# Optimization experiments

Measured on AMD Instinct MI355X. Metric: run time of the kernel, lower is better.

Reference implementation:

```python
import jax, jax.numpy as jnp
import numpy as np

B, S, H, W, DF, D, HID, ITERS = 8, 8, 64, 64, 64, 64, 128, 3
EPS = 1e-8


def build_grid(h, w):
    ranges = [np.linspace(-1.0, 1.0, num=h), np.linspace(-1.0, 1.0, num=w)]
    g = np.meshgrid(*ranges, sparse=False, indexing='xy')
    return jnp.asarray(np.stack(g, axis=-1), dtype=jnp.float32)  # [H, W, 2]


def ln(x, g, b):
    m = jnp.mean(x, axis=-1, keepdims=True)
    v = jnp.mean((x - m) ** 2, axis=-1, keepdims=True)
    return (x - m) * jax.lax.rsqrt(v + 1e-5) * g + b


def setup_inputs() -> dict:
    key = jax.random.key(0)
    ks = iter(jax.random.split(key, 64))
    def nrm(shape, s=0.02):
        return jax.random.normal(next(ks), shape, jnp.float32) * s
    inp = {}
    inp['inputs'] = jax.random.normal(next(ks), (B, H, W, DF), jnp.float32)
    # learned slot inits and learned per-slot position / scale factors
    inp['slots_p'] = jax.random.normal(next(ks), (1, S, D), jnp.float32)
    inp['s_pos_p'] = 2.0 * jax.random.uniform(next(ks), (1, S, 2), jnp.float32) - 1.0
    inp['s_scale_p'] = 0.1 + 0.01 * jax.random.normal(next(ks), (1, S, 2), jnp.float32)
    # soft position embedding Linear(2, D)
    inp['W_pos'] = nrm((2, D)); inp['b_pos'] = jnp.zeros((D,), jnp.float32)
    # q/k/v projections
    inp['Wq'] = nrm((D, D)); inp['bq'] = jnp.zeros((D,), jnp.float32)
    inp['Wk'] = nrm((DF, D)); inp['bk'] = jnp.zeros((D,), jnp.float32)
    inp['Wv'] = nrm((DF, D)); inp['bv'] = jnp.zeros((D,), jnp.float32)
    # layernorms
    inp['g_in'] = jnp.ones((DF,), jnp.float32); inp['b_in'] = jnp.zeros((DF,), jnp.float32)
    inp['g_slots'] = jnp.ones((D,), jnp.float32); inp['b_slots'] = jnp.zeros((D,), jnp.float32)
    inp['g_k'] = jnp.ones((D,), jnp.float32); inp['b_k'] = jnp.zeros((D,), jnp.float32)
    inp['g_v'] = jnp.ones((D,), jnp.float32); inp['b_v'] = jnp.zeros((D,), jnp.float32)
    # shared kv MLP fc1_kv / fc2_kv
    inp['W1'] = nrm((D, 2 * D)); inp['b1'] = jnp.zeros((2 * D,), jnp.float32)
    inp['W2'] = nrm((2 * D, D)); inp['b2'] = jnp.zeros((D,), jnp.float32)
    # GRUCell (torch layout transposed to [in, 3*D])
    inp['W_ih'] = nrm((D, 3 * D)); inp['b_ih'] = jnp.zeros((3 * D,), jnp.float32)
    inp['W_hh'] = nrm((D, 3 * D)); inp['b_hh'] = jnp.zeros((3 * D,), jnp.float32)
    # residual slot MLP
    inp['g_pre'] = jnp.ones((D,), jnp.float32); inp['b_pre'] = jnp.zeros((D,), jnp.float32)
    inp['Wf1'] = nrm((D, HID)); inp['bf1'] = jnp.zeros((HID,), jnp.float32)
    inp['Wf2'] = nrm((HID, D)); inp['bf2'] = jnp.zeros((D,), jnp.float32)
    return inp


def reference(inputs, slots_p, s_pos_p, s_scale_p, W_pos, b_pos, Wq, bq, Wk, bk, Wv, bv,
              g_in, b_in, g_slots, b_slots, g_k, b_k, g_v, b_v, W1, b1, W2, b2,
              W_ih, W_hh, b_ih, b_hh, g_pre, b_pre, Wf1, bf1, Wf2, bf2):
    grid = build_grid(H, W)                 # [H, W, 2]
    grid_flat = grid.reshape(-1, 2)          # [HW, 2]
    scale = D ** (-0.5)

    x = ln(inputs, g_in, b_in)
    k0 = x @ Wk + bk                         # [B, H, W, D]
    v0 = x @ Wv + bv

    slots = jnp.broadcast_to(slots_p, (B, S, D))
    s_pos = jnp.clip(jnp.broadcast_to(s_pos_p, (B, S, 2)), -1.0, 1.0)[:, :, None, None, :]
    s_scale = jnp.clip(jnp.broadcast_to(s_scale_p, (B, S, 2)), 1e-3, 2.0)[:, :, None, None, :]

    def proj_kv(base, sp, ss, g, b):
        gr = (grid[None, None] - sp) / (ss * 5.0)      # [B, S, H, W, 2]
        pe = gr @ W_pos + b_pos                        # [B, S, H, W, D]
        t = (base[:, None] + pe).reshape(B, S, H * W, D)
        t = ln(t, g, b)
        return jax.nn.relu(t @ W1 + b1) @ W2 + b2      # [B, S, HW, D]

    for i in range(ITERS + 1):
        slots_prev = slots
        q = ln(slots, g_slots, b_slots) @ Wq + bq       # [B, S, D]
        kk = proj_kv(k0, s_pos, s_scale, g_k, b_k)
        vv = proj_kv(v0, s_pos, s_scale, g_v, b_v)
        dots = jnp.einsum('bid,bijd->bij', q, kk) * scale
        attn_mask = jax.nn.softmax(dots, axis=1) + EPS  # softmax over slot axis
        attn = attn_mask / jnp.sum(attn_mask, axis=-1, keepdims=True)
        updates = jnp.einsum('bijd,bij->bid', vv, attn)
        if i < ITERS:
            xg = updates.reshape(-1, D) @ W_ih + b_ih
            hg = slots_prev.reshape(-1, D) @ W_hh + b_hh
            ir, iz, inn = jnp.split(xg, 3, axis=-1)
            hr, hz, hn = jnp.split(hg, 3, axis=-1)
            r = jax.nn.sigmoid(ir + hr)
            z = jax.nn.sigmoid(iz + hz)
            n = jnp.tanh(inn + r * hn)
            slots = ((1.0 - z) * n + z * slots_prev.reshape(-1, D)).reshape(B, S, D)
            slots = slots + (jax.nn.relu(ln(slots, g_pre, b_pre) @ Wf1 + bf1) @ Wf2 + bf2)
        else:
            slots = slots_prev
        # update per-slot position / scale from the attention mask
        sp = jnp.einsum('bij,jd->bid', attn_mask, grid_flat) / jnp.sum(attn_mask, axis=-1, keepdims=True)
        diff = grid_flat[None, None] - sp[:, :, None]   # [B, S, HW, 2]
        am = attn_mask + 1e-8
        ss = jnp.sqrt(jnp.einsum('bij,bijd->bid', am, diff ** 2) / jnp.sum(am, axis=-1, keepdims=True))
        s_pos = sp[:, :, None, None, :]
        s_scale = jnp.clip(ss, 1e-3, 2.0)[:, :, None, None, :]
    return slots, s_pos, s_scale, attn_mask
```

## Files before the change

### kernel.cpp

```cpp
#include <hip/hip_runtime.h>
#include <math.h>

typedef __bf16 bf16_t;
typedef __bf16 bfrag __attribute__((ext_vector_type(8)));
typedef float ffrag __attribute__((ext_vector_type(4)));

__device__ __forceinline__ float wave_sum(float v) {
#pragma unroll
  for (int m = 32; m >= 1; m >>= 1) v += __shfl_xor(v, m, 64);
  return v;
}
__device__ __forceinline__ float lin_(int i) { return -1.f + (2.f * (float)i) / 63.f; }
__device__ __forceinline__ float bflo(unsigned u) { return __uint_as_float(u << 16); }
__device__ __forceinline__ float bfhi(unsigned u) { return __uint_as_float(u & 0xFFFF0000u); }

__global__ __launch_bounds__(256) void k_setup(
    const float* __restrict__ slots_p, const float* __restrict__ s_pos_p,
    const float* __restrict__ s_scale_p, const float* __restrict__ W1,
    const float* __restrict__ b1, const float* __restrict__ g_k,
    const float* __restrict__ b_k, const float* __restrict__ g_v,
    const float* __restrict__ b_v, const float* __restrict__ W_pos,
    const float* __restrict__ b_pos, const float* __restrict__ Wk,
    const float* __restrict__ Wv,
    float* __restrict__ slotsS, float* __restrict__ sposS,
    float* __restrict__ sscaleS, float* __restrict__ momentsHsum,
    bf16_t* __restrict__ W1kT, bf16_t* __restrict__ W1vT,
    bf16_t* __restrict__ WkT, bf16_t* __restrict__ WvT,
    float4* __restrict__ nckA, float* __restrict__ nckB,
    float4* __restrict__ ncvA, float* __restrict__ ncvB,
    float* __restrict__ possum) {
  int t = threadIdx.x;
  for (int i = t; i < 8512; i += 256) momentsHsum[i] = 0.f;
  for (int i = t; i < 4096; i += 256) slotsS[i] = slots_p[i & 511];
  if (t < 128) {
    sposS[t] = fminf(fmaxf(s_pos_p[t & 15], -1.f), 1.f);
    sscaleS[t] = fminf(fmaxf(s_scale_p[t & 15], 0.001f), 2.f);
  }
  for (int i = t; i < 4096; i += 256) {
    int n = i >> 6, d = i & 63;
    WkT[i] = (bf16_t)Wk[d * 64 + n];
    WvT[i] = (bf16_t)Wv[d * 64 + n];
  }
  if (t < 128) {
    int n = t;
    float wxk = 0, wyk = 0, wbk = 0, uk = 0, sk = 0;
    float wxv = 0, wyv = 0, wbv = 0, uv = 0, sv = 0;
    for (int c = 0; c < 64; ++c) {
      float w = W1[c * 128 + n];
      float wk = g_k[c] * w, wv = g_v[c] * w;
      W1kT[n * 64 + c] = (bf16_t)wk;
      W1vT[n * 64 + c] = (bf16_t)wv;
      float px = W_pos[c], py = W_pos[64 + c], bp = b_pos[c];
      wxk += px * wk; wyk += py * wk; wbk += bp * wk; sk += wk; uk += b_k[c] * w;
      wxv += px * wv; wyv += py * wv; wbv += bp * wv; sv += wv; uv += b_v[c] * w;
    }
    nckA[n] = make_float4(wxk, wyk, wbk, uk + b1[n]); nckB[n] = sk;
    ncvA[n] = make_float4(wxv, wyv, wbv, uv + b1[n]); ncvB[n] = sv;
  }
  if (t < 64) {
    float px = W_pos[t], py = W_pos[64 + t], bp = b_pos[t];
    float s[9] = {px, py, bp, px * px, py * py, bp * bp, px * py, px * bp, py * bp};
#pragma unroll
    for (int i = 0; i < 9; ++i) {
      float v = wave_sum(s[i]);
      if (t == 0) possum[i] = v;
    }
  }
}

__device__ __forceinline__ void pass_type(
    const bf16_t xs[][72], bf16_t t0s[][72],
    const bf16_t WTl[][72], const bf16_t W1l[][72],
    const float* __restrict__ bias, const float* wpxs, const float* wpys,
    const float* bpvs, float* __restrict__ statsG, bf16_t* __restrict__ P0G,
    int j0, int wv, int lq, int ln15) {
  ffrag C[4] = {{0,0,0,0},{0,0,0,0},{0,0,0,0},{0,0,0,0}};
#pragma unroll
  for (int ks = 0; ks < 2; ++ks) {
    bfrag a = *(const bfrag*)&xs[wv * 16 + ln15][ks * 32 + lq * 8];
#pragma unroll
    for (int nt = 0; nt < 4; ++nt) {
      bfrag bb = *(const bfrag*)&WTl[nt * 16 + ln15][ks * 32 + lq * 8];
      C[nt] = __builtin_amdgcn_mfma_f32_16x16x32_bf16(a, bb, C[nt], 0, 0, 0);
    }
  }
  float kv[4][4];
  float st[5][4];
#pragma unroll
  for (int i = 0; i < 5; ++i)
#pragma unroll
    for (int rg = 0; rg < 4; ++rg) st[i][rg] = 0.f;
#pragma unroll
  for (int nt = 0; nt < 4; ++nt) {
    int n = nt * 16 + ln15;
    float bn = bias[n], pxw = wpxs[n], pyw = wpys[n], bpw = bpvs[n];
#pragma unroll
    for (int rg = 0; rg < 4; ++rg) {
      float v = C[nt][rg] + bn;
      kv[nt][rg] = v;
      st[0][rg] += v; st[1][rg] += v * v; st[2][rg] += v * pxw;
      st[3][rg] += v * pyw; st[4][rg] += v * bpw;
    }
  }
#pragma unroll
  for (int i = 0; i < 5; ++i)
#pragma unroll
    for (int rg = 0; rg < 4; ++rg) {
      float v = st[i][rg];
      v += __shfl_xor(v, 1, 64); v += __shfl_xor(v, 2, 64);
      v += __shfl_xor(v, 4, 64); v += __shfl_xor(v, 8, 64);
      st[i][rg] = v;
    }
  if (ln15 == 0) {
#pragma unroll
    for (int rg = 0; rg < 4; ++rg) {
      int j = j0 + wv * 16 + lq * 4 + rg;
#pragma unroll
      for (int i = 0; i < 5; ++i) statsG[j * 5 + i] = st[i][rg];
    }
  }
#pragma unroll
  for (int nt = 0; nt < 4; ++nt)
#pragma unroll
    for (int rg = 0; rg < 4; ++rg)
      t0s[wv * 16 + lq * 4 + rg][nt * 16 + ln15] = (bf16_t)kv[nt][rg];
  ffrag D[8] = {{0,0,0,0},{0,0,0,0},{0,0,0,0},{0,0,0,0},
                {0,0,0,0},{0,0,0,0},{0,0,0,0},{0,0,0,0}};
#pragma unroll
  for (int ks = 0; ks < 2; ++ks) {
    bfrag a = *(const bfrag*)&t0s[wv * 16 + ln15][ks * 32 + lq * 8];
#pragma unroll
    for (int nt = 0; nt < 8; ++nt) {
      bfrag bb = *(const bfrag*)&W1l[nt * 16 + ln15][ks * 32 + lq * 8];
      D[nt] = __builtin_amdgcn_mfma_f32_16x16x32_bf16(a, bb, D[nt], 0, 0, 0);
    }
  }
#pragma unroll
  for (int nt = 0; nt < 8; ++nt)
#pragma unroll
    for (int rg = 0; rg < 4; ++rg)
      P0G[(size_t)(j0 + wv * 16 + lq * 4 + rg) * 128 + nt * 16 + ln15] =
          (bf16_t)D[nt][rg];
}

__global__ __launch_bounds__(256) void k_pre(
    const float* __restrict__ inp, const float* __restrict__ g_in,
    const float* __restrict__ b_in, const float* __restrict__ bk,
    const float* __restrict__ bv, const bf16_t* __restrict__ WkT,
    const bf16_t* __restrict__ WvT, const bf16_t* __restrict__ W1kT,
    const bf16_t* __restrict__ W1vT, const float* __restrict__ W_pos,
    const float* __restrict__ b_pos,
    bf16_t* __restrict__ P0k, bf16_t* __restrict__ P0v,
    float* __restrict__ statsK, float* __restrict__ statsV,
    const float* __restrict__ slotsS, const float* __restrict__ g_slots,
    const float* __restrict__ b_slots, const float* __restrict__ Wq,
    const float* __restrict__ bq, const float* __restrict__ W2,
    const float* __restrict__ b2, float* __restrict__ w2qg,
    float* __restrict__ b2qg) {
  __shared__ bf16_t xs[64][72];
  __shared__ bf16_t t0s[64][72];
  __shared__ bf16_t WkTl[64][72];
  __shared__ bf16_t WvTl[64][72];
  __shared__ bf16_t W1kl[128][72];
  __shared__ bf16_t W1vl[128][72];
  __shared__ float wpxs[64], wpys[64], bpvs[64];
  const int tid = threadIdx.x;
  const int j0 = blockIdx.x * 64;
  for (int i = tid; i < 512; i += 256) {
    int row = i >> 3, seg = i & 7;
    *(uint4*)&WkTl[row][seg * 8] = ((const uint4*)WkT)[i];
    *(uint4*)&WvTl[row][seg * 8] = ((const uint4*)WvT)[i];
  }
  for (int i = tid; i < 1024; i += 256) {
    int row = i >> 3, seg = i & 7;
    *(uint4*)&W1kl[row][seg * 8] = ((const uint4*)W1kT)[i];
    *(uint4*)&W1vl[row][seg * 8] = ((const uint4*)W1vT)[i];
  }
  if (tid < 64) { wpxs[tid] = W_pos[tid]; wpys[tid] = W_pos[64 + tid]; bpvs[tid] = b_pos[tid]; }
  {
    const int px = tid >> 2, cg = tid & 3;
    const float* rowp = inp + (size_t)(j0 + px) * 64 + cg * 16;
    float v[16];
    *(float4*)&v[0]  = ((const float4*)rowp)[0];
    *(float4*)&v[4]  = ((const float4*)rowp)[1];
    *(float4*)&v[8]  = ((const float4*)rowp)[2];
    *(float4*)&v[12] = ((const float4*)rowp)[3];
    float s = 0.f, s2 = 0.f;
#pragma unroll
    for (int i = 0; i < 16; ++i) { s += v[i]; s2 += v[i] * v[i]; }
    s += __shfl_xor(s, 1, 64); s += __shfl_xor(s, 2, 64);
    s2 += __shfl_xor(s2, 1, 64); s2 += __shfl_xor(s2, 2, 64);
    float m = s * 0.015625f;
    float r = rsqrtf(s2 * 0.015625f - m * m + 1e-5f);
    float g[16], bb[16];
    *(float4*)&g[0]  = ((const float4*)(g_in + cg * 16))[0];
    *(float4*)&g[4]  = ((const float4*)(g_in + cg * 16))[1];
    *(float4*)&g[8]  = ((const float4*)(g_in + cg * 16))[2];
    *(float4*)&g[12] = ((const float4*)(g_in + cg * 16))[3];
    *(float4*)&bb[0]  = ((const float4*)(b_in + cg * 16))[0];
    *(float4*)&bb[4]  = ((const float4*)(b_in + cg * 16))[1];
    *(float4*)&bb[8]  = ((const float4*)(b_in + cg * 16))[2];
    *(float4*)&bb[12] = ((const float4*)(b_in + cg * 16))[3];
#pragma unroll
    for (int e = 0; e < 8; ++e) {
      float x0 = (v[2 * e] - m) * r * g[2 * e] + bb[2 * e];
      float x1 = (v[2 * e + 1] - m) * r * g[2 * e + 1] + bb[2 * e + 1];
      union { unsigned u; bf16_t h[2]; } cv;
      cv.h[0] = (bf16_t)x0; cv.h[1] = (bf16_t)x1;
      *(unsigned*)&xs[px][cg * 16 + 2 * e] = cv.u;
    }
  }
  __syncthreads();
  const int wv = tid >> 6, lane = tid & 63, lq = lane >> 4, ln15 = lane & 15;
  pass_type(xs, t0s, WkTl, W1kl, bk, wpxs, wpys, bpvs, statsK, P0k, j0, wv, lq, ln15);
  pass_type(xs, t0s, WvTl, W1vl, bv, wpxs, wpys, bpvs, statsV, P0v, j0, wv, lq, ln15);
  if (blockIdx.x < 64 && tid < 64) {
    int bs = blockIdx.x, d = tid;
    float v = slotsS[bs * 64 + d];
    float m = wave_sum(v) * 0.015625f;
    float c = v - m;
    float var = wave_sum(c * c) * 0.015625f;
    float xn = c * rsqrtf(var + 1e-5f) * g_slots[d] + b_slots[d];
    float q = bq[d];
    for (int cc = 0; cc < 64; ++cc) q = fmaf(__shfl(xn, cc, 64), Wq[cc * 64 + d], q);
    float w0 = 0.f, w1 = 0.f;
    for (int cc = 0; cc < 64; ++cc) {
      float qc = __shfl(q, cc, 64);
      w0 = fmaf(W2[d * 64 + cc], qc, w0);
      w1 = fmaf(W2[(64 + d) * 64 + cc], qc, w1);
    }
    w2qg[bs * 128 + d] = w0;
    w2qg[bs * 128 + 64 + d] = w1;
    float p = wave_sum(b2[d] * q);
    if (d == 0) b2qg[bs] = p;
  }
}

template <int LAST>
__global__ __launch_bounds__(256) void k_iter(
    const bf16_t* __restrict__ P0kg, const bf16_t* __restrict__ P0vg,
    const float* __restrict__ statsK, const float* __restrict__ statsV,
    const float4* __restrict__ nckA, const float* __restrict__ nckB,
    const float4* __restrict__ ncvA, const float* __restrict__ ncvB,
    const float* __restrict__ possum, const float* __restrict__ w2qg,
    const float* __restrict__ b2qg, const float* __restrict__ sposS,
    const float* __restrict__ sscaleS, float* __restrict__ moments,
    float* __restrict__ Hsum, float* __restrict__ outAttn) {
  __shared__ unsigned P0kl[64 * 65];
  __shared__ unsigned P0vl[64 * 65];
  __shared__ float4 nckAl[128];
  __shared__ float nckBl[128];
  __shared__ float w2qTl[128][8];
  __shared__ float4 scalV[64][9];
  __shared__ float attnS[64][10];
  __shared__ float HsumW[4][8][128];
  __shared__ float momAcc[8][5];
  const int tid = threadIdx.x;
  const int tile = blockIdx.x, b = blockIdx.y;
  const int jg0 = b * 4096 + tile * 64;
#pragma unroll
  for (int r = 0; r < 4; ++r) {
    int idx = tid + 256 * r;
    int row = idx >> 4, seg = idx & 15;
    uint4 v = ((const uint4*)P0kg)[(size_t)(jg0 + row) * 16 + seg];
    unsigned* dst = &P0kl[row * 65 + seg * 4];
    dst[0] = v.x; dst[1] = v.y; dst[2] = v.z; dst[3] = v.w;
    if (!LAST) {
      uint4 w = ((const uint4*)P0vg)[(size_t)(jg0 + row) * 16 + seg];
      unsigned* d2 = &P0vl[row * 65 + seg * 4];
      d2[0] = w.x; d2[1] = w.y; d2[2] = w.z; d2[3] = w.w;
    }
  }
  if (tid < 128) { nckAl[tid] = nckA[tid]; nckBl[tid] = nckB[tid]; }
#pragma unroll
  for (int r = 0; r < 4; ++r) {
    int idx = tid + 256 * r;
    int s = idx >> 7, n = idx & 127;
    w2qTl[n][s] = w2qg[(b * 8 + s) * 128 + n];
  }
  if (tid < 40) momAcc[tid / 5][tid % 5] = 0.f;
  float4 ncv0 = {0, 0, 0, 0}, ncv1 = {0, 0, 0, 0};
  float wsv0 = 0.f, wsv1 = 0.f;
  if (!LAST) {
    int l = tid & 63;
    ncv0 = ncvA[l]; ncv1 = ncvA[l + 64];
    wsv0 = ncvB[l]; wsv1 = ncvB[l + 64];
  }
  __syncthreads();

  const int px = tid >> 2, sp = tid & 3;
  const int jimg = tile * 64 + px;
  const float gx = lin_(jimg & 63), gy = lin_(jimg >> 6);
  const float Swx = possum[0], Swy = possum[1], Sbp = possum[2];
  const float Swx2 = possum[3], Swy2 = possum[4], Sbp2 = possum[5];
  const float Swxy = possum[6], Swxb = possum[7], Swyb = possum[8];
  float skA[5], svA[5];
#pragma unroll
  for (int i = 0; i < 5; ++i) {
    skA[i] = statsK[(size_t)(jg0 + px) * 5 + i];
    svA[i] = statsV[(size_t)(jg0 + px) * 5 + i];
  }
  float c1a[8], c2a[8], rKa[8], mrKa[8];
#pragma unroll
  for (int s = 0; s < 8; ++s) {
    int bs = b * 8 + s;
    float spx = sposS[bs * 2], spy = sposS[bs * 2 + 1];
    float rxx = 1.f / (sscaleS[bs * 2] * 5.f);
    float ryy = 1.f / (sscaleS[bs * 2 + 1] * 5.f);
    float c1 = (gx - spx) * rxx, c2 = (gy - spy) * ryy;
    float quad = c1 * c1 * Swx2 + c2 * c2 * Swy2 + Sbp2 +
                 2.f * (c1 * c2 * Swxy + c1 * Swxb + c2 * Swyb);
    float mK = (skA[0] + c1 * Swx + c2 * Swy + Sbp) * 0.015625f;
    float e2K = (skA[1] + 2.f * (c1 * skA[2] + c2 * skA[3] + skA[4]) + quad) * 0.015625f;
    float rK = rsqrtf(e2K - mK * mK + 1e-5f);
    c1a[s] = c1; c2a[s] = c2; rKa[s] = rK; mrKa[s] = mK * rK;
    if (!LAST && (s >> 1) == sp) {
      float mV = (svA[0] + c1 * Swx + c2 * Swy + Sbp) * 0.015625f;
      float e2V = (svA[1] + 2.f * (c1 * svA[2] + c2 * svA[3] + svA[4]) + quad) * 0.015625f;
      float rV = rsqrtf(e2V - mV * mV + 1e-5f);
      scalV[px][s] = make_float4(c1, c2, rV, mV * rV);
    }
  }
  float d8[8] = {0, 0, 0, 0, 0, 0, 0, 0};
#pragma unroll 4
  for (int i = 0; i < 16; ++i) {
    int k = sp * 16 + i;
    unsigned u = P0kl[px * 65 + k];
    float p0 = bflo(u), p1 = bfhi(u);
    float4 A0 = nckAl[2 * k], A1 = nckAl[2 * k + 1];
    float ws0 = nckBl[2 * k], ws1 = nckBl[2 * k + 1];
    float4 q0a = *(const float4*)&w2qTl[2 * k][0];
    float4 q0b = *(const float4*)&w2qTl[2 * k][4];
    float4 q1a = *(const float4*)&w2qTl[2 * k + 1][0];
    float4 q1b = *(const float4*)&w2qTl[2 * k + 1][4];
    float qq0[8] = {q0a.x, q0a.y, q0a.z, q0a.w, q0b.x, q0b.y, q0b.z, q0b.w};
    float qq1[8] = {q1a.x, q1a.y, q1a.z, q1a.w, q1b.x, q1b.y, q1b.z, q1b.w};
    float bm0 = p0 + A0.z, bm1 = p1 + A1.z;
#pragma unroll
    for (int s = 0; s < 8; ++s) {
      float z0 = bm0 + c1a[s] * A0.x + c2a[s] * A0.y;
      float h0 = fmaxf(fmaf(rKa[s], z0, fmaf(-mrKa[s], ws0, A0.w)), 0.f);
      d8[s] = fmaf(h0, qq0[s], d8[s]);
      float z1 = bm1 + c1a[s] * A1.x + c2a[s] * A1.y;
      float h1 = fmaxf(fmaf(rKa[s], z1, fmaf(-mrKa[s], ws1, A1.w)), 0.f);
      d8[s] = fmaf(h1, qq1[s], d8[s]);
    }
  }
#pragma unroll
  for (int s = 0; s < 8; ++s) {
    float v = d8[s];
    v += __shfl_xor(v, 1, 64);
    v += __shfl_xor(v, 2, 64);
    d8[s] = (v + b2qg[b * 8 + s]) * 0.125f;
  }
  float mx = d8[0];
#pragma unroll
  for (int s = 1; s < 8; ++s) mx = fmaxf(mx, d8[s]);
  float tt = 0.f;
  float e8[8];
#pragma unroll
  for (int s = 0; s < 8; ++s) { e8[s] = expf(d8[s] - mx); tt += e8[s]; }
  float inv = 1.f / tt;
#pragma unroll
  for (int s = 0; s < 8; ++s) e8[s] = e8[s] * inv + 1e-8f;
  float wa, wb;
  if (sp == 0) { wa = e8[0]; wb = e8[1]; }
  else if (sp == 1) { wa = e8[2]; wb = e8[3]; }
  else if (sp == 2) { wa = e8[4]; wb = e8[5]; }
  else { wa = e8[6]; wb = e8[7]; }
  *(float2*)&attnS[px][sp * 2] = make_float2(wa, wb);
  if (LAST) {
    outAttn[(size_t)(b * 8 + sp * 2) * 4096 + jimg] = wa;
    outAttn[(size_t)(b * 8 + sp * 2 + 1) * 4096 + jimg] = wb;
  }
  {
    float mm[10] = {wa, wa * gx, wa * gy, wa * gx * gx, wa * gy * gy,
                    wb, wb * gx, wb * gy, wb * gx * gx, wb * gy * gy};
#pragma unroll
    for (int i = 0; i < 10; ++i) {
      float v = mm[i];
      v += __shfl_xor(v, 4, 64); v += __shfl_xor(v, 8, 64);
      v += __shfl_xor(v, 16, 64); v += __shfl_xor(v, 32, 64);
      mm[i] = v;
    }
    if ((tid & 63) < 4) {
#pragma unroll
      for (int i = 0; i < 5; ++i) {
        atomicAdd(&momAcc[sp * 2][i], mm[i]);
        atomicAdd(&momAcc[sp * 2 + 1][i], mm[5 + i]);
      }
    }
  }
  __syncthreads();

  if (!LAST) {
    const int w = tid >> 6, l = tid & 63;
    float hacc[8][2];
#pragma unroll
    for (int s = 0; s < 8; ++s) { hacc[s][0] = 0.f; hacc[s][1] = 0.f; }
    const unsigned short* P16 = (const unsigned short*)P0vl;
#pragma unroll 2
    for (int i = 0; i < 16; ++i) {
      int j = w * 16 + i;
      float pv0 = __uint_as_float((unsigned)P16[j * 130 + l] << 16);
      float pv1 = __uint_as_float((unsigned)P16[j * 130 + 64 + l] << 16);
      float bm0 = pv0 + ncv0.z, bm1 = pv1 + ncv1.z;
#pragma unroll
      for (int s = 0; s < 8; ++s) {
        float4 sc = scalV[j][s];
        float aw = attnS[j][s];
        float z0 = bm0 + sc.x * ncv0.x + sc.y * ncv0.y;
        float h0 = fmaxf(fmaf(sc.z, z0, fmaf(-sc.w, wsv0, ncv0.w)), 0.f);
        hacc[s][0] = fmaf(aw, h0, hacc[s][0]);
        float z1 = bm1 + sc.x * ncv1.x + sc.y * ncv1.y;
        float h1 = fmaxf(fmaf(sc.z, z1, fmaf(-sc.w, wsv1, ncv1.w)), 0.f);
        hacc[s][1] = fmaf(aw, h1, hacc[s][1]);
      }
    }
#pragma unroll
    for (int s = 0; s < 8; ++s) {
      HsumW[w][s][l] = hacc[s][0];
      HsumW[w][s][l + 64] = hacc[s][1];
    }
    __syncthreads();
#pragma unroll
    for (int r = 0; r < 4; ++r) {
      int i = tid + 256 * r;
      int s = i >> 7, n = i & 127;
      float v = HsumW[0][s][n] + HsumW[1][s][n] + HsumW[2][s][n] + HsumW[3][s][n];
      atomicAdd(&Hsum[(b * 8 + s) * 128 + n], v);
    }
  }
  if (tid < 40)
    atomicAdd(&moments[(b * 8 + tid / 5) * 5 + tid % 5], momAcc[tid / 5][tid % 5]);
}

__global__ __launch_bounds__(192) void k_fin(
    float* __restrict__ moments, float* __restrict__ Hsum,
    const float* __restrict__ W2, const float* __restrict__ b2,
    const float* __restrict__ W_ih, const float* __restrict__ b_ih,
    const float* __restrict__ W_hh, const float* __restrict__ b_hh,
    const float* __restrict__ g_pre, const float* __restrict__ b_pre,
    const float* __restrict__ Wf1, const float* __restrict__ bf1,
    const float* __restrict__ Wf2, const float* __restrict__ bf2,
    const float* __restrict__ g_slots, const float* __restrict__ b_slots,
    const float* __restrict__ Wq, const float* __restrict__ bq,
    float* __restrict__ slotsS, float* __restrict__ sposS, float* __restrict__ sscaleS,
    float* __restrict__ w2qg, float* __restrict__ b2qg,
    float* __restrict__ outSlots, float* __restrict__ outSpos,
    float* __restrict__ outSscale, int last) {
  const int bs = blockIdx.x;
  const int t = threadIdx.x;
  __shared__ float hsum_s[128], upd[64], sprev[64], xg[192], hg[192];
  __shared__ float snew[64], xpre[64], hf[128], sfin[64], xn[64], qsh[64];
  const float M0 = moments[bs * 5 + 0];
  const float M1x = moments[bs * 5 + 1], M1y = moments[bs * 5 + 2];
  const float M2x = moments[bs * 5 + 3], M2y = moments[bs * 5 + 4];
  const float invM0 = 1.f / M0;
  const float spx = M1x * invM0, spy = M1y * invM0;
  const float M0a = M0 + 4096.f * 1e-8f;
  const float G2 = 1408.6772487f * 1e-8f;
  const float vx = (M2x + G2 - 2.f * spx * M1x + spx * spx * M0a) / M0a;
  const float vy = (M2y + G2 - 2.f * spy * M1y + spy * spy * M0a) / M0a;
  float ssx = sqrtf(fmaxf(vx, 0.f)), ssy = sqrtf(fmaxf(vy, 0.f));
  ssx = fminf(fmaxf(ssx, 0.001f), 2.f);
  ssy = fminf(fmaxf(ssy, 0.001f), 2.f);
  if (t == 0) {
    sposS[bs * 2 + 0] = spx; sposS[bs * 2 + 1] = spy;
    sscaleS[bs * 2 + 0] = ssx; sscaleS[bs * 2 + 1] = ssy;
    if (last) {
      outSpos[bs * 2 + 0] = spx; outSpos[bs * 2 + 1] = spy;
      outSscale[bs * 2 + 0] = ssx; outSscale[bs * 2 + 1] = ssy;
    }
  }
  if (last) {
    if (t < 64) outSlots[bs * 64 + t] = slotsS[bs * 64 + t];
    return;
  }
  if (t < 128) hsum_s[t] = Hsum[bs * 128 + t];
  if (t < 64) sprev[t] = slotsS[bs * 64 + t];
  __syncthreads();
  if (t < 128) Hsum[bs * 128 + t] = 0.f;
  if (t < 5) moments[bs * 5 + t] = 0.f;
  if (t < 64) {
    float a = 0.f;
#pragma unroll
    for (int k = 0; k < 128; ++k) a += hsum_s[k] * W2[k * 64 + t];
    upd[t] = a * invM0 + b2[t];
  }
  __syncthreads();
  {
    float a = b_ih[t], h = b_hh[t];
#pragma unroll
    for (int d = 0; d < 64; ++d) {
      a += upd[d] * W_ih[d * 192 + t];
      h += sprev[d] * W_hh[d * 192 + t];
    }
    xg[t] = a; hg[t] = h;
  }
  __syncthreads();
  if (t < 64) {
    float r = 1.f / (1.f + expf(-(xg[t] + hg[t])));
    float z = 1.f / (1.f + expf(-(xg[64 + t] + hg[64 + t])));
    float n = tanhf(xg[128 + t] + r * hg[128 + t]);
    snew[t] = (1.f - z) * n + z * sprev[t];
  }
  __syncthreads();
  if (t < 64) {
    float v = snew[t];
    float m = wave_sum(v) * 0.015625f;
    float c = v - m;
    float var = wave_sum(c * c) * 0.015625f;
    xpre[t] = c * rsqrtf(var + 1e-5f) * g_pre[t] + b_pre[t];
  }
  __syncthreads();
  if (t < 128) {
    float a = bf1[t];
#pragma unroll
    for (int d = 0; d < 64; ++d) a += xpre[d] * Wf1[d * 128 + t];
    hf[t] = fmaxf(a, 0.f);
  }
  __syncthreads();
  if (t < 64) {
    float a = bf2[t];
#pragma unroll
    for (int k = 0; k < 128; ++k) a += hf[k] * Wf2[k * 64 + t];
    float nv = snew[t] + a;
    slotsS[bs * 64 + t] = nv;
    sfin[t] = nv;
  }
  __syncthreads();
  if (t < 64) {
    float v = sfin[t];
    float m = wave_sum(v) * 0.015625f;
    float c = v - m;
    float var = wave_sum(c * c) * 0.015625f;
    xn[t] = c * rsqrtf(var + 1e-5f) * g_slots[t] + b_slots[t];
  }
  __syncthreads();
  if (t < 64) {
    float a = bq[t];
#pragma unroll
    for (int d = 0; d < 64; ++d) a += xn[d] * Wq[d * 64 + t];
    qsh[t] = a;
  }
  __syncthreads();
  if (t < 128) {
    float a = 0.f;
#pragma unroll
    for (int d = 0; d < 64; ++d) a += W2[t * 64 + d] * qsh[d];
    w2qg[bs * 128 + t] = a;
  }
  if (t < 64) {
    float p = wave_sum(b2[t] * qsh[t]);
    if (t == 0) b2qg[bs] = p;
  }
}

extern "C" void kernel_launch(void* const* d_in, const int* in_sizes, int n_in,
                              void* d_out, int out_size, void* d_ws, size_t ws_size,
                              hipStream_t stream) {
  const float* const* in = (const float* const*)d_in;
  float* ws = (float*)d_ws;
  bf16_t* P0k   = (bf16_t*)(ws + 0);
  bf16_t* P0v   = (bf16_t*)(ws + 2097152);
  float* statsK = ws + 4194304;
  float* statsV = ws + 4358144;
  float* w2qg   = ws + 4521984;
  float* b2qg   = ws + 4530176;
  float* slotsS = ws + 4530240;
  float* sposS  = ws + 4534336;
  float* sscaleS= ws + 4534464;
  float* moments= ws + 4534592;
  float* Hsum   = ws + 4534912;
  bf16_t* W1kT  = (bf16_t*)(ws + 4543104);
  bf16_t* W1vT  = (bf16_t*)(ws + 4547200);
  bf16_t* WkT   = (bf16_t*)(ws + 4551296);
  bf16_t* WvT   = (bf16_t*)(ws + 4553344);
  float4* nckA  = (float4*)(ws + 4555392);
  float* nckB   = ws + 4555904;
  float4* ncvA  = (float4*)(ws + 4556032);
  float* ncvB   = ws + 4556544;
  float* possum = ws + 4556672;

  float* out = (float*)d_out;
  float* outSlots  = out;
  float* outSpos   = out + 4096;
  float* outSscale = out + 4224;
  float* outAttn   = out + 4352;

  k_setup<<<1, 256, 0, stream>>>(in[1], in[2], in[3], in[20], in[21],
                                 in[16], in[17], in[18], in[19], in[4], in[5],
                                 in[8], in[10], slotsS, sposS, sscaleS, moments,
                                 W1kT, W1vT, WkT, WvT, nckA, nckB, ncvA, ncvB, possum);
  k_pre<<<512, 256, 0, stream>>>(in[0], in[12], in[13], in[9], in[11],
                                 WkT, WvT, W1kT, W1vT, in[4], in[5],
                                 P0k, P0v, statsK, statsV,
                                 slotsS, in[14], in[15], in[6], in[7], in[22], in[23],
                                 w2qg, b2qg);
  for (int i = 0; i < 4; ++i) {
    int last = (i == 3) ? 1 : 0;
    if (!last) {
      k_iter<0><<<dim3(64, 8), 256, 0, stream>>>(
          P0k, P0v, statsK, statsV, nckA, nckB, ncvA, ncvB, possum,
          w2qg, b2qg, sposS, sscaleS, moments, Hsum, outAttn);
    } else {
      k_iter<1><<<dim3(64, 8), 256, 0, stream>>>(
          P0k, P0v, statsK, statsV, nckA, nckB, ncvA, ncvB, possum,
          w2qg, b2qg, sposS, sscaleS, moments, Hsum, outAttn);
    }
    k_fin<<<64, 192, 0, stream>>>(moments, Hsum, in[22], in[23], in[24], in[25],
                                  in[26], in[27], in[28], in[29], in[30], in[31],
                                  in[32], in[33], in[14], in[15], in[6], in[7],
                                  slotsS, sposS, sscaleS, w2qg, b2qg,
                                  outSlots, outSpos, outSscale, last);
  }
}
```

Measured before the change: 300.4 us.

## Fuse setup, precompute and iteration kernels into one persistent kernel with grid barriers

Replaces the chain of setup, pre, iter and fin launches with a single persistent kernel of 256 blocks synchronised by atomic-counter grid barriers. Each block keeps its two tiles of projected K/V activations (P0k/P0v) and per-row stats in shared memory across all iterations, instead of writing them to global memory and reading them back. This removes about ten kernel launches and the global round trips of the large intermediate buffers. In exchange it relies on all blocks being co-resident, uses about 118 KB of shared memory per block, and leaves the tiny finalize step serialised on 64 blocks while the others wait at the barrier.

```diff
diff --git a/kernel.cpp b/kernel.cpp
--- a/kernel.cpp
+++ b/kernel.cpp
@@ -4,6 +4,8 @@
 typedef __bf16 bf16_t;
 typedef __bf16 bfrag __attribute__((ext_vector_type(8)));
 typedef float ffrag __attribute__((ext_vector_type(4)));
+
+#define NBLK 256u
 
 __device__ __forceinline__ float wave_sum(float v) {
 #pragma unroll
@@ -14,66 +16,53 @@
 __device__ __forceinline__ float bflo(unsigned u) { return __uint_as_float(u << 16); }
 __device__ __forceinline__ float bfhi(unsigned u) { return __uint_as_float(u & 0xFFFF0000u); }
 
-__global__ __launch_bounds__(256) void k_setup(
-    const float* __restrict__ slots_p, const float* __restrict__ s_pos_p,
-    const float* __restrict__ s_scale_p, const float* __restrict__ W1,
-    const float* __restrict__ b1, const float* __restrict__ g_k,
-    const float* __restrict__ b_k, const float* __restrict__ g_v,
-    const float* __restrict__ b_v, const float* __restrict__ W_pos,
-    const float* __restrict__ b_pos, const float* __restrict__ Wk,
-    const float* __restrict__ Wv,
-    float* __restrict__ slotsS, float* __restrict__ sposS,
-    float* __restrict__ sscaleS, float* __restrict__ momentsHsum,
-    bf16_t* __restrict__ W1kT, bf16_t* __restrict__ W1vT,
-    bf16_t* __restrict__ WkT, bf16_t* __restrict__ WvT,
-    float4* __restrict__ nckA, float* __restrict__ nckB,
-    float4* __restrict__ ncvA, float* __restrict__ ncvB,
-    float* __restrict__ possum) {
-  int t = threadIdx.x;
-  for (int i = t; i < 8512; i += 256) momentsHsum[i] = 0.f;
-  for (int i = t; i < 4096; i += 256) slotsS[i] = slots_p[i & 511];
-  if (t < 128) {
-    sposS[t] = fminf(fmaxf(s_pos_p[t & 15], -1.f), 1.f);
-    sscaleS[t] = fminf(fmaxf(s_scale_p[t & 15], 0.001f), 2.f);
-  }
-  for (int i = t; i < 4096; i += 256) {
-    int n = i >> 6, d = i & 63;
-    WkT[i] = (bf16_t)Wk[d * 64 + n];
-    WvT[i] = (bf16_t)Wv[d * 64 + n];
-  }
-  if (t < 128) {
-    int n = t;
-    float wxk = 0, wyk = 0, wbk = 0, uk = 0, sk = 0;
-    float wxv = 0, wyv = 0, wbv = 0, uv = 0, sv = 0;
-    for (int c = 0; c < 64; ++c) {
-      float w = W1[c * 128 + n];
-      float wk = g_k[c] * w, wv = g_v[c] * w;
-      W1kT[n * 64 + c] = (bf16_t)wk;
-      W1vT[n * 64 + c] = (bf16_t)wv;
-      float px = W_pos[c], py = W_pos[64 + c], bp = b_pos[c];
-      wxk += px * wk; wyk += py * wk; wbk += bp * wk; sk += wk; uk += b_k[c] * w;
-      wxv += px * wv; wyv += py * wv; wbv += bp * wv; sv += wv; uv += b_v[c] * w;
-    }
-    nckA[n] = make_float4(wxk, wyk, wbk, uk + b1[n]); nckB[n] = sk;
-    ncvA[n] = make_float4(wxv, wyv, wbv, uv + b1[n]); ncvB[n] = sv;
-  }
-  if (t < 64) {
-    float px = W_pos[t], py = W_pos[64 + t], bp = b_pos[t];
-    float s[9] = {px, py, bp, px * px, py * py, bp * bp, px * py, px * bp, py * bp};
-#pragma unroll
-    for (int i = 0; i < 9; ++i) {
-      float v = wave_sum(s[i]);
-      if (t == 0) possum[i] = v;
-    }
-  }
+__device__ __forceinline__ void gbar(unsigned* ctr) {
+  __syncthreads();
+  if (threadIdx.x == 0) {
+    __threadfence();
+    atomicAdd(ctr, 1u);
+    while (__hip_atomic_load(ctr, __ATOMIC_RELAXED, __HIP_MEMORY_SCOPE_AGENT) < NBLK)
+      __builtin_amdgcn_s_sleep(1);
+  }
+  __syncthreads();
+  __threadfence();
 }
 
+struct FinS {
+  float hsum_s[128], upd[64], sprev[64], xg[192], hg[192];
+  float snew[64], xpre[64], hf[128], sfin[64], xn[64], qsh[64];
+};
+struct SmemPre {
+  bf16_t xs[64][72];
+  bf16_t t0s[64][72];
+  bf16_t WTl[64][72];
+  bf16_t W1l[128][72];
+  float wpxs[64], wpys[64], bpvs[64];
+};
+struct SmemIter {
+  float4 nckAl[128];
+  float nckBl[128];
+  float w2qTl[128][8];
+  float4 scalV[64][9];
+  float attnS[64][10];
+  union { float HsumW[4][8][128]; FinS fin; };
+  float momAcc[8][5];
+};
+struct Smem {
+  unsigned P0kl[2][64 * 65];
+  unsigned P0vl[2][64 * 65];
+  float scr[2][640];
+  union { SmemPre pre; SmemIter it; } u;
+};
+static_assert(sizeof(Smem) == 118528, "layout");
+static_assert(sizeof(Smem) <= 163840, "fits one block per CU");
+
 __device__ __forceinline__ void pass_type(
-    const bf16_t xs[][72], bf16_t t0s[][72],
-    const bf16_t WTl[][72], const bf16_t W1l[][72],
+    const bf16_t (*xs)[72], bf16_t (*t0s)[72],
+    const bf16_t (*WTl)[72], const bf16_t (*W1l)[72],
     const float* __restrict__ bias, const float* wpxs, const float* wpys,
-    const float* bpvs, float* __restrict__ statsG, bf16_t* __restrict__ P0G,
-    int j0, int wv, int lq, int ln15) {
+    const float* bpvs, float st[5][4], unsigned* P0L,
+    int wv, int lq, int ln15) {
   ffrag C[4] = {{0,0,0,0},{0,0,0,0},{0,0,0,0},{0,0,0,0}};
 #pragma unroll
   for (int ks = 0; ks < 2; ++ks) {
@@ -85,7 +74,6 @@
     }
   }
   float kv[4][4];
-  float st[5][4];
 #pragma unroll
   for (int i = 0; i < 5; ++i)
 #pragma unroll
@@ -111,14 +99,6 @@
       v += __shfl_xor(v, 4, 64); v += __shfl_xor(v, 8, 64);
       st[i][rg] = v;
     }
-  if (ln15 == 0) {
-#pragma unroll
-    for (int rg = 0; rg < 4; ++rg) {
-      int j = j0 + wv * 16 + lq * 4 + rg;
-#pragma unroll
-      for (int i = 0; i < 5; ++i) statsG[j * 5 + i] = st[i][rg];
-    }
-  }
 #pragma unroll
   for (int nt = 0; nt < 4; ++nt)
 #pragma unroll
@@ -135,94 +115,218 @@
       D[nt] = __builtin_amdgcn_mfma_f32_16x16x32_bf16(a, bb, D[nt], 0, 0, 0);
     }
   }
+  bf16_t* P16 = (bf16_t*)P0L;
 #pragma unroll
   for (int nt = 0; nt < 8; ++nt)
 #pragma unroll
     for (int rg = 0; rg < 4; ++rg)
-      P0G[(size_t)(j0 + wv * 16 + lq * 4 + rg) * 128 + nt * 16 + ln15] =
-          (bf16_t)D[nt][rg];
+      P16[(wv * 16 + lq * 4 + rg) * 130 + nt * 16 + ln15] = (bf16_t)D[nt][rg];
 }
 
-__global__ __launch_bounds__(256) void k_pre(
-    const float* __restrict__ inp, const float* __restrict__ g_in,
-    const float* __restrict__ b_in, const float* __restrict__ bk,
-    const float* __restrict__ bv, const bf16_t* __restrict__ WkT,
-    const bf16_t* __restrict__ WvT, const bf16_t* __restrict__ W1kT,
-    const bf16_t* __restrict__ W1vT, const float* __restrict__ W_pos,
+__global__ __launch_bounds__(256) void k_fused(
+    const float* __restrict__ inp,
+    const float* __restrict__ slots_p,
+    const float* __restrict__ s_pos_p,
+    const float* __restrict__ s_scale_p,
+    const float* __restrict__ W_pos,
     const float* __restrict__ b_pos,
-    bf16_t* __restrict__ P0k, bf16_t* __restrict__ P0v,
-    float* __restrict__ statsK, float* __restrict__ statsV,
-    const float* __restrict__ slotsS, const float* __restrict__ g_slots,
-    const float* __restrict__ b_slots, const float* __restrict__ Wq,
-    const float* __restrict__ bq, const float* __restrict__ W2,
-    const float* __restrict__ b2, float* __restrict__ w2qg,
-    float* __restrict__ b2qg) {
-  __shared__ bf16_t xs[64][72];
-  __shared__ bf16_t t0s[64][72];
-  __shared__ bf16_t WkTl[64][72];
-  __shared__ bf16_t WvTl[64][72];
-  __shared__ bf16_t W1kl[128][72];
-  __shared__ bf16_t W1vl[128][72];
-  __shared__ float wpxs[64], wpys[64], bpvs[64];
+    const float* __restrict__ Wq,
+    const float* __restrict__ bq,
+    const float* __restrict__ Wk,
+    const float* __restrict__ bk,
+    const float* __restrict__ Wv,
+    const float* __restrict__ bv,
+    const float* __restrict__ g_in,
+    const float* __restrict__ b_in,
+    const float* __restrict__ g_slots,
+    const float* __restrict__ b_slots,
+    const float* __restrict__ g_k,
+    const float* __restrict__ b_k,
+    const float* __restrict__ g_v,
+    const float* __restrict__ b_v,
+    const float* __restrict__ W1,
+    const float* __restrict__ b1,
+    const float* __restrict__ W2,
+    const float* __restrict__ b2,
+    const float* __restrict__ W_ih,
+    const float* __restrict__ b_ih,
+    const float* __restrict__ W_hh,
+    const float* __restrict__ b_hh,
+    const float* __restrict__ g_pre,
+    const float* __restrict__ b_pre,
+    const float* __restrict__ Wf1,
+    const float* __restrict__ bf1,
+    const float* __restrict__ Wf2,
+    const float* __restrict__ bf2,
+    float* __restrict__ ws,
+    float* __restrict__ outSlots, float* __restrict__ outSpos,
+    float* __restrict__ outSscale, float* __restrict__ outAttn) {
+  __shared__ Smem sm;
   const int tid = threadIdx.x;
-  const int j0 = blockIdx.x * 64;
-  for (int i = tid; i < 512; i += 256) {
-    int row = i >> 3, seg = i & 7;
-    *(uint4*)&WkTl[row][seg * 8] = ((const uint4*)WkT)[i];
-    *(uint4*)&WvTl[row][seg * 8] = ((const uint4*)WvT)[i];
-  }
-  for (int i = tid; i < 1024; i += 256) {
-    int row = i >> 3, seg = i & 7;
-    *(uint4*)&W1kl[row][seg * 8] = ((const uint4*)W1kT)[i];
-    *(uint4*)&W1vl[row][seg * 8] = ((const uint4*)W1vT)[i];
-  }
-  if (tid < 64) { wpxs[tid] = W_pos[tid]; wpys[tid] = W_pos[64 + tid]; bpvs[tid] = b_pos[tid]; }
-  {
-    const int px = tid >> 2, cg = tid & 3;
-    const float* rowp = inp + (size_t)(j0 + px) * 64 + cg * 16;
-    float v[16];
-    *(float4*)&v[0]  = ((const float4*)rowp)[0];
-    *(float4*)&v[4]  = ((const float4*)rowp)[1];
-    *(float4*)&v[8]  = ((const float4*)rowp)[2];
-    *(float4*)&v[12] = ((const float4*)rowp)[3];
-    float s = 0.f, s2 = 0.f;
-#pragma unroll
-    for (int i = 0; i < 16; ++i) { s += v[i]; s2 += v[i] * v[i]; }
-    s += __shfl_xor(s, 1, 64); s += __shfl_xor(s, 2, 64);
-    s2 += __shfl_xor(s2, 1, 64); s2 += __shfl_xor(s2, 2, 64);
-    float m = s * 0.015625f;
-    float r = rsqrtf(s2 * 0.015625f - m * m + 1e-5f);
-    float g[16], bb[16];
-    *(float4*)&g[0]  = ((const float4*)(g_in + cg * 16))[0];
-    *(float4*)&g[4]  = ((const float4*)(g_in + cg * 16))[1];
-    *(float4*)&g[8]  = ((const float4*)(g_in + cg * 16))[2];
-    *(float4*)&g[12] = ((const float4*)(g_in + cg * 16))[3];
-    *(float4*)&bb[0]  = ((const float4*)(b_in + cg * 16))[0];
-    *(float4*)&bb[4]  = ((const float4*)(b_in + cg * 16))[1];
-    *(float4*)&bb[8]  = ((const float4*)(b_in + cg * 16))[2];
-    *(float4*)&bb[12] = ((const float4*)(b_in + cg * 16))[3];
-#pragma unroll
-    for (int e = 0; e < 8; ++e) {
-      float x0 = (v[2 * e] - m) * r * g[2 * e] + bb[2 * e];
-      float x1 = (v[2 * e + 1] - m) * r * g[2 * e + 1] + bb[2 * e + 1];
-      union { unsigned u; bf16_t h[2]; } cv;
-      cv.h[0] = (bf16_t)x0; cv.h[1] = (bf16_t)x1;
-      *(unsigned*)&xs[px][cg * 16 + 2 * e] = cv.u;
-    }
-  }
-  __syncthreads();
+  const int bid = blockIdx.x;
+  const int tl = bid & 63;
+  const int b0 = bid >> 6;
+
+  float* slotsS  = ws;
+  float* sposS   = ws + 4096;
+  float* sscaleS = ws + 4224;
+  float* moments = ws + 4352;
+  float* Hsum    = ws + 4672;
+  float* w2qg    = ws + 12864;
+  float* b2qg    = ws + 21056;
+  bf16_t* W1kT   = (bf16_t*)(ws + 21120);
+  bf16_t* W1vT   = (bf16_t*)(ws + 25216);
+  bf16_t* WkT    = (bf16_t*)(ws + 29312);
+  bf16_t* WvT    = (bf16_t*)(ws + 31360);
+  float4* nckA   = (float4*)(ws + 33408);
+  float* nckB    = ws + 33920;
+  float4* ncvA   = (float4*)(ws + 34048);
+  float* ncvB    = ws + 34560;
+  float* possum  = ws + 34688;
+  unsigned* bar  = (unsigned*)(ws + 34816);
+
+  if (bid == 0) {
+    int t = tid;
+    for (int i = t; i < 8512; i += 256) moments[i] = 0.f;
+    for (int i = t; i < 4096; i += 256) slotsS[i] = slots_p[i & 511];
+    if (t < 128) {
+      sposS[t] = fminf(fmaxf(s_pos_p[t & 15], -1.f), 1.f);
+      sscaleS[t] = fminf(fmaxf(s_scale_p[t & 15], 0.001f), 2.f);
+    }
+    for (int i = t; i < 4096; i += 256) {
+      int n = i >> 6, d = i & 63;
+      WkT[i] = (bf16_t)Wk[d * 64 + n];
+      WvT[i] = (bf16_t)Wv[d * 64 + n];
+    }
+    if (t < 128) {
+      int n = t;
+      float wxk = 0, wyk = 0, wbk = 0, uk = 0, sk = 0;
+      float wxv = 0, wyv = 0, wbv = 0, uv = 0, sv = 0;
+      for (int c = 0; c < 64; ++c) {
+        float w = W1[c * 128 + n];
+        float wkk = g_k[c] * w, wvv = g_v[c] * w;
+        W1kT[n * 64 + c] = (bf16_t)wkk;
+        W1vT[n * 64 + c] = (bf16_t)wvv;
+        float pxc = W_pos[c], pyc = W_pos[64 + c], bpc = b_pos[c];
+        wxk += pxc * wkk; wyk += pyc * wkk; wbk += bpc * wkk; sk += wkk; uk += b_k[c] * w;
+        wxv += pxc * wvv; wyv += pyc * wvv; wbv += bpc * wvv; sv += wvv; uv += b_v[c] * w;
+      }
+      nckA[n] = make_float4(wxk, wyk, wbk, uk + b1[n]); nckB[n] = sk;
+      ncvA[n] = make_float4(wxv, wyv, wbv, uv + b1[n]); ncvB[n] = sv;
+    }
+    if (t < 64) {
+      float pxc = W_pos[t], pyc = W_pos[64 + t], bpc = b_pos[t];
+      float s9[9] = {pxc, pyc, bpc, pxc * pxc, pyc * pyc, bpc * bpc,
+                     pxc * pyc, pxc * bpc, pyc * bpc};
+#pragma unroll
+      for (int i = 0; i < 9; ++i) {
+        float v = wave_sum(s9[i]);
+        if (t == 0) possum[i] = v;
+      }
+    }
+  }
+  gbar(&bar[0]);
+
   const int wv = tid >> 6, lane = tid & 63, lq = lane >> 4, ln15 = lane & 15;
-  pass_type(xs, t0s, WkTl, W1kl, bk, wpxs, wpys, bpvs, statsK, P0k, j0, wv, lq, ln15);
-  pass_type(xs, t0s, WvTl, W1vl, bv, wpxs, wpys, bpvs, statsV, P0v, j0, wv, lq, ln15);
-  if (blockIdx.x < 64 && tid < 64) {
-    int bs = blockIdx.x, d = tid;
+  for (int u = 0; u < 2; ++u) {
+    const int j0 = (bid + u * 256) * 64;
+    {
+      const int pxl = tid >> 2, cgl = tid & 3;
+      const float* rowp = inp + (size_t)(j0 + pxl) * 64 + cgl * 16;
+      float v[16];
+      *(float4*)&v[0]  = ((const float4*)rowp)[0];
+      *(float4*)&v[4]  = ((const float4*)rowp)[1];
+      *(float4*)&v[8]  = ((const float4*)rowp)[2];
+      *(float4*)&v[12] = ((const float4*)rowp)[3];
+      float s = 0.f, s2 = 0.f;
+#pragma unroll
+      for (int i = 0; i < 16; ++i) { s += v[i]; s2 += v[i] * v[i]; }
+      s += __shfl_xor(s, 1, 64); s += __shfl_xor(s, 2, 64);
+      s2 += __shfl_xor(s2, 1, 64); s2 += __shfl_xor(s2, 2, 64);
+      float m = s * 0.015625f;
+      float r = rsqrtf(s2 * 0.015625f - m * m + 1e-5f);
+      float g[16], bb[16];
+      *(float4*)&g[0]  = ((const float4*)(g_in + cgl * 16))[0];
+      *(float4*)&g[4]  = ((const float4*)(g_in + cgl * 16))[1];
+      *(float4*)&g[8]  = ((const float4*)(g_in + cgl * 16))[2];
+      *(float4*)&g[12] = ((const float4*)(g_in + cgl * 16))[3];
+      *(float4*)&bb[0]  = ((const float4*)(b_in + cgl * 16))[0];
+      *(float4*)&bb[4]  = ((const float4*)(b_in + cgl * 16))[1];
+      *(float4*)&bb[8]  = ((const float4*)(b_in + cgl * 16))[2];
+      *(float4*)&bb[12] = ((const float4*)(b_in + cgl * 16))[3];
+#pragma unroll
+      for (int e = 0; e < 8; ++e) {
+        float x0 = (v[2 * e] - m) * r * g[2 * e] + bb[2 * e];
+        float x1 = (v[2 * e + 1] - m) * r * g[2 * e + 1] + bb[2 * e + 1];
+        union { unsigned uu; bf16_t h[2]; } cv;
+        cv.h[0] = (bf16_t)x0; cv.h[1] = (bf16_t)x1;
+        *(unsigned*)&sm.u.pre.xs[pxl][cgl * 16 + 2 * e] = cv.uu;
+      }
+    }
+    if (u == 0 && tid < 64) {
+      sm.u.pre.wpxs[tid] = W_pos[tid];
+      sm.u.pre.wpys[tid] = W_pos[64 + tid];
+      sm.u.pre.bpvs[tid] = b_pos[tid];
+    }
+    for (int i = tid; i < 512; i += 256) {
+      int row = i >> 3, seg = i & 7;
+      *(uint4*)&sm.u.pre.WTl[row][seg * 8] = ((const uint4*)WkT)[i];
+    }
+    for (int i = tid; i < 1024; i += 256) {
+      int row = i >> 3, seg = i & 7;
+      *(uint4*)&sm.u.pre.W1l[row][seg * 8] = ((const uint4*)W1kT)[i];
+    }
+    __syncthreads();
+    float stK[5][4], stV[5][4];
+    pass_type(sm.u.pre.xs, sm.u.pre.t0s, sm.u.pre.WTl, sm.u.pre.W1l, bk,
+              sm.u.pre.wpxs, sm.u.pre.wpys, sm.u.pre.bpvs, stK, sm.P0kl[u],
+              wv, lq, ln15);
+    __syncthreads();
+    for (int i = tid; i < 512; i += 256) {
+      int row = i >> 3, seg = i & 7;
+      *(uint4*)&sm.u.pre.WTl[row][seg * 8] = ((const uint4*)WvT)[i];
+    }
+    for (int i = tid; i < 1024; i += 256) {
+      int row = i >> 3, seg = i & 7;
+      *(uint4*)&sm.u.pre.W1l[row][seg * 8] = ((const uint4*)W1vT)[i];
+    }
+    __syncthreads();
+    pass_type(sm.u.pre.xs, sm.u.pre.t0s, sm.u.pre.WTl, sm.u.pre.W1l, bv,
+              sm.u.pre.wpxs, sm.u.pre.wpys, sm.u.pre.bpvs, stV, sm.P0vl[u],
+              wv, lq, ln15);
+    if (ln15 == 0) {
+#pragma unroll
+      for (int rg = 0; rg < 4; ++rg) {
+        int row = wv * 16 + lq * 4 + rg;
+#pragma unroll
+        for (int i = 0; i < 5; ++i) {
+          sm.scr[u][row * 5 + i] = stK[i][rg];
+          sm.scr[u][320 + row * 5 + i] = stV[i][rg];
+        }
+      }
+    }
+    __syncthreads();
+  }
+
+  if (tid < 128) { sm.u.it.nckAl[tid] = nckA[tid]; sm.u.it.nckBl[tid] = nckB[tid]; }
+  float4 ncv0, ncv1; float wsv0, wsv1;
+  { int l = tid & 63; ncv0 = ncvA[l]; ncv1 = ncvA[l + 64]; wsv0 = ncvB[l]; wsv1 = ncvB[l + 64]; }
+  const float Swx = possum[0], Swy = possum[1], Sbp = possum[2];
+  const float Swx2 = possum[3], Swy2 = possum[4], Sbp2 = possum[5];
+  const float Swxy = possum[6], Swxb = possum[7], Swyb = possum[8];
+  const int px = tid >> 2, sp = tid & 3;
+  const int jimg = tl * 64 + px;
+  const float gx = lin_(px), gy = lin_(tl);
+
+  if (bid < 64 && tid < 64) {
+    int bs = bid, d = tid;
     float v = slotsS[bs * 64 + d];
     float m = wave_sum(v) * 0.015625f;
     float c = v - m;
     float var = wave_sum(c * c) * 0.015625f;
-    float xn = c * rsqrtf(var + 1e-5f) * g_slots[d] + b_slots[d];
+    float xnv = c * rsqrtf(var + 1e-5f) * g_slots[d] + b_slots[d];
     float q = bq[d];
-    for (int cc = 0; cc < 64; ++cc) q = fmaf(__shfl(xn, cc, 64), Wq[cc * 64 + d], q);
+    for (int cc = 0; cc < 64; ++cc) q = fmaf(__shfl(xnv, cc, 64), Wq[cc * 64 + d], q);
     float w0 = 0.f, w1 = 0.f;
     for (int cc = 0; cc < 64; ++cc) {
       float qc = __shfl(q, cc, 64);
@@ -234,385 +338,297 @@
     float p = wave_sum(b2[d] * q);
     if (d == 0) b2qg[bs] = p;
   }
-}
-
-template <int LAST>
-__global__ __launch_bounds__(256) void k_iter(
-    const bf16_t* __restrict__ P0kg, const bf16_t* __restrict__ P0vg,
-    const float* __restrict__ statsK, const float* __restrict__ statsV,
-    const float4* __restrict__ nckA, const float* __restrict__ nckB,
-    const float4* __restrict__ ncvA, const float* __restrict__ ncvB,
-    const float* __restrict__ possum, const float* __restrict__ w2qg,
-    const float* __restrict__ b2qg, const float* __restrict__ sposS,
-    const float* __restrict__ sscaleS, float* __restrict__ moments,
-    float* __restrict__ Hsum, float* __restrict__ outAttn) {
-  __shared__ unsigned P0kl[64 * 65];
-  __shared__ unsigned P0vl[64 * 65];
-  __shared__ float4 nckAl[128];
-  __shared__ float nckBl[128];
-  __shared__ float w2qTl[128][8];
-  __shared__ float4 scalV[64][9];
-  __shared__ float attnS[64][10];
-  __shared__ float HsumW[4][8][128];
-  __shared__ float momAcc[8][5];
-  const int tid = threadIdx.x;
-  const int tile = blockIdx.x, b = blockIdx.y;
-  const int jg0 = b * 4096 + tile * 64;
-#pragma unroll
-  for (int r = 0; r < 4; ++r) {
-    int idx = tid + 256 * r;
-    int row = idx >> 4, seg = idx & 15;
-    uint4 v = ((const uint4*)P0kg)[(size_t)(jg0 + row) * 16 + seg];
-    unsigned* dst = &P0kl[row * 65 + seg * 4];
-    dst[0] = v.x; dst[1] = v.y; dst[2] = v.z; dst[3] = v.w;
-    if (!LAST) {
-      uint4 w = ((const uint4*)P0vg)[(size_t)(jg0 + row) * 16 + seg];
-      unsigned* d2 = &P0vl[row * 65 + seg * 4];
-      d2[0] = w.x; d2[1] = w.y; d2[2] = w.z; d2[3] = w.w;
-    }
-  }
-  if (tid < 128) { nckAl[tid] = nckA[tid]; nckBl[tid] = nckB[tid]; }
-#pragma unroll
-  for (int r = 0; r < 4; ++r) {
-    int idx = tid + 256 * r;
-    int s = idx >> 7, n = idx & 127;
-    w2qTl[n][s] = w2qg[(b * 8 + s) * 128 + n];
-  }
-  if (tid < 40) momAcc[tid / 5][tid % 5] = 0.f;
-  float4 ncv0 = {0, 0, 0, 0}, ncv1 = {0, 0, 0, 0};
-  float wsv0 = 0.f, wsv1 = 0.f;
-  if (!LAST) {
-    int l = tid & 63;
-    ncv0 = ncvA[l]; ncv1 = ncvA[l + 64];
-    wsv0 = ncvB[l]; wsv1 = ncvB[l + 64];
-  }
-  __syncthreads();
-
-  const int px = tid >> 2, sp = tid & 3;
-  const int jimg = tile * 64 + px;
-  const float gx = lin_(jimg & 63), gy = lin_(jimg >> 6);
-  const float Swx = possum[0], Swy = possum[1], Sbp = possum[2];
-  const float Swx2 = possum[3], Swy2 = possum[4], Sbp2 = possum[5];
-  const float Swxy = possum[6], Swxb = possum[7], Swyb = possum[8];
-  float skA[5], svA[5];
-#pragma unroll
-  for (int i = 0; i < 5; ++i) {
-    skA[i] = statsK[(size_t)(jg0 + px) * 5 + i];
-    svA[i] = statsV[(size_t)(jg0 + px) * 5 + i];
-  }
-  float c1a[8], c2a[8], rKa[8], mrKa[8];
-#pragma unroll
-  for (int s = 0; s < 8; ++s) {
-    int bs = b * 8 + s;
-    float spx = sposS[bs * 2], spy = sposS[bs * 2 + 1];
-    float rxx = 1.f / (sscaleS[bs * 2] * 5.f);
-    float ryy = 1.f / (sscaleS[bs * 2 + 1] * 5.f);
-    float c1 = (gx - spx) * rxx, c2 = (gy - spy) * ryy;
-    float quad = c1 * c1 * Swx2 + c2 * c2 * Swy2 + Sbp2 +
-                 2.f * (c1 * c2 * Swxy + c1 * Swxb + c2 * Swyb);
-    float mK = (skA[0] + c1 * Swx + c2 * Swy + Sbp) * 0.015625f;
-    float e2K = (skA[1] + 2.f * (c1 * skA[2] + c2 * skA[3] + skA[4]) + quad) * 0.015625f;
-    float rK = rsqrtf(e2K - mK * mK + 1e-5f);
-    c1a[s] = c1; c2a[s] = c2; rKa[s] = rK; mrKa[s] = mK * rK;
-    if (!LAST && (s >> 1) == sp) {
-      float mV = (svA[0] + c1 * Swx + c2 * Swy + Sbp) * 0.015625f;
-      float e2V = (svA[1] + 2.f * (c1 * svA[2] + c2 * svA[3] + svA[4]) + quad) * 0.015625f;
-      float rV = rsqrtf(e2V - mV * mV + 1e-5f);
-      scalV[px][s] = make_float4(c1, c2, rV, mV * rV);
-    }
-  }
-  float d8[8] = {0, 0, 0, 0, 0, 0, 0, 0};
+
+  for (int itn = 0; itn < 4; ++itn) {
+    const int last = (itn == 3);
+    gbar(&bar[(1 + 2 * itn) * 16]);
+
+#pragma unroll
+    for (int u = 0; u < 2; ++u) {
+      const int b_u = b0 + 4 * u;
+#pragma unroll
+      for (int r = 0; r < 4; ++r) {
+        int idx = tid + 256 * r;
+        int s = idx >> 7, n = idx & 127;
+        sm.u.it.w2qTl[n][s] = w2qg[(b_u * 8 + s) * 128 + n];
+      }
+      if (tid < 40) sm.u.it.momAcc[tid / 5][tid % 5] = 0.f;
+      __syncthreads();
+
+      float skA[5], svA[5];
+#pragma unroll
+      for (int i = 0; i < 5; ++i) {
+        skA[i] = sm.scr[u][px * 5 + i];
+        svA[i] = sm.scr[u][320 + px * 5 + i];
+      }
+      float c1a[8], c2a[8], rKa[8], mrKa[8];
+#pragma unroll
+      for (int s = 0; s < 8; ++s) {
+        int bs = b_u * 8 + s;
+        float spx = sposS[bs * 2], spy = sposS[bs * 2 + 1];
+        float rxx = 1.f / (sscaleS[bs * 2] * 5.f);
+        float ryy = 1.f / (sscaleS[bs * 2 + 1] * 5.f);
+        float c1 = (gx - spx) * rxx, c2 = (gy - spy) * ryy;
+        float quad = c1 * c1 * Swx2 + c2 * c2 * Swy2 + Sbp2 +
+                     2.f * (c1 * c2 * Swxy + c1 * Swxb + c2 * Swyb);
+        float mK = (skA[0] + c1 * Swx + c2 * Swy + Sbp) * 0.015625f;
+        float e2K = (skA[1] + 2.f * (c1 * skA[2] + c2 * skA[3] + skA[4]) + quad) * 0.015625f;
+        float rK = rsqrtf(e2K - mK * mK + 1e-5f);
+        c1a[s] = c1; c2a[s] = c2; rKa[s] = rK; mrKa[s] = mK * rK;
+        if (!last && (s >> 1) == sp) {
+          float mV = (svA[0] + c1 * Swx + c2 * Swy + Sbp) * 0.015625f;
+          float e2V = (svA[1] + 2.f * (c1 * svA[2] + c2 * svA[3] + svA[4]) + quad) * 0.015625f;
+          float rV = rsqrtf(e2V - mV * mV + 1e-5f);
+          sm.u.it.scalV[px][s] = make_float4(c1, c2, rV, mV * rV);
+        }
+      }
+      float d8[8] = {0, 0, 0, 0, 0, 0, 0, 0};
 #pragma unroll 4
-  for (int i = 0; i < 16; ++i) {
-    int k = sp * 16 + i;
-    unsigned u = P0kl[px * 65 + k];
-    float p0 = bflo(u), p1 = bfhi(u);
-    float4 A0 = nckAl[2 * k], A1 = nckAl[2 * k + 1];
-    float ws0 = nckBl[2 * k], ws1 = nckBl[2 * k + 1];
-    float4 q0a = *(const float4*)&w2qTl[2 * k][0];
-    float4 q0b = *(const float4*)&w2qTl[2 * k][4];
-    float4 q1a = *(const float4*)&w2qTl[2 * k + 1][0];
-    float4 q1b = *(const float4*)&w2qTl[2 * k + 1][4];
-    float qq0[8] = {q0a.x, q0a.y, q0a.z, q0a.w, q0b.x, q0b.y, q0b.z, q0b.w};
-    float qq1[8] = {q1a.x, q1a.y, q1a.z, q1a.w, q1b.x, q1b.y, q1b.z, q1b.w};
-    float bm0 = p0 + A0.z, bm1 = p1 + A1.z;
-#pragma unroll
-    for (int s = 0; s < 8; ++s) {
-      float z0 = bm0 + c1a[s] * A0.x + c2a[s] * A0.y;
-      float h0 = fmaxf(fmaf(rKa[s], z0, fmaf(-mrKa[s], ws0, A0.w)), 0.f);
-      d8[s] = fmaf(h0, qq0[s], d8[s]);
-      float z1 = bm1 + c1a[s] * A1.x + c2a[s] * A1.y;
-      float h1 = fmaxf(fmaf(rKa[s], z1, fmaf(-mrKa[s], ws1, A1.w)), 0.f);
-      d8[s] = fmaf(h1, qq1[s], d8[s]);
-    }
-  }
-#pragma unroll
-  for (int s = 0; s < 8; ++s) {
-    float v = d8[s];
-    v += __shfl_xor(v, 1, 64);
-    v += __shfl_xor(v, 2, 64);
-    d8[s] = (v + b2qg[b * 8 + s]) * 0.125f;
-  }
-  float mx = d8[0];
-#pragma unroll
-  for (int s = 1; s < 8; ++s) mx = fmaxf(mx, d8[s]);
-  float tt = 0.f;
-  float e8[8];
-#pragma unroll
-  for (int s = 0; s < 8; ++s) { e8[s] = expf(d8[s] - mx); tt += e8[s]; }
-  float inv = 1.f / tt;
-#pragma unroll
-  for (int s = 0; s < 8; ++s) e8[s] = e8[s] * inv + 1e-8f;
-  float wa, wb;
-  if (sp == 0) { wa = e8[0]; wb = e8[1]; }
-  else if (sp == 1) { wa = e8[2]; wb = e8[3]; }
-  else if (sp == 2) { wa = e8[4]; wb = e8[5]; }
-  else { wa = e8[6]; wb = e8[7]; }
-  *(float2*)&attnS[px][sp * 2] = make_float2(wa, wb);
-  if (LAST) {
-    outAttn[(size_t)(b * 8 + sp * 2) * 4096 + jimg] = wa;
-    outAttn[(size_t)(b * 8 + sp * 2 + 1) * 4096 + jimg] = wb;
-  }
-  {
-    float mm[10] = {wa, wa * gx, wa * gy, wa * gx * gx, wa * gy * gy,
-                    wb, wb * gx, wb * gy, wb * gx * gx, wb * gy * gy};
-#pragma unroll
-    for (int i = 0; i < 10; ++i) {
-      float v = mm[i];
-      v += __shfl_xor(v, 4, 64); v += __shfl_xor(v, 8, 64);
-      v += __shfl_xor(v, 16, 64); v += __shfl_xor(v, 32, 64);
-      mm[i] = v;
-    }
-    if ((tid & 63) < 4) {
-#pragma unroll
-      for (int i = 0; i < 5; ++i) {
-        atomicAdd(&momAcc[sp * 2][i], mm[i]);
-        atomicAdd(&momAcc[sp * 2 + 1][i], mm[5 + i]);
-      }
-    }
-  }
-  __syncthreads();
-
-  if (!LAST) {
-    const int w = tid >> 6, l = tid & 63;
-    float hacc[8][2];
-#pragma unroll
-    for (int s = 0; s < 8; ++s) { hacc[s][0] = 0.f; hacc[s][1] = 0.f; }
-    const unsigned short* P16 = (const unsigned short*)P0vl;
+      for (int i = 0; i < 16; ++i) {
+        int k = sp * 16 + i;
+        unsigned uu = sm.P0kl[u][px * 65 + k];
+        float p0 = bflo(uu), p1 = bfhi(uu);
+        float4 A0 = sm.u.it.nckAl[2 * k], A1 = sm.u.it.nckAl[2 * k + 1];
+        float ws0 = sm.u.it.nckBl[2 * k], ws1 = sm.u.it.nckBl[2 * k + 1];
+        float4 q0a = *(const float4*)&sm.u.it.w2qTl[2 * k][0];
+        float4 q0b = *(const float4*)&sm.u.it.w2qTl[2 * k][4];
+        float4 q1a = *(const float4*)&sm.u.it.w2qTl[2 * k + 1][0];
+        float4 q1b = *(const float4*)&sm.u.it.w2qTl[2 * k + 1][4];
+        float qq0[8] = {q0a.x, q0a.y, q0a.z, q0a.w, q0b.x, q0b.y, q0b.z, q0b.w};
+        float qq1[8] = {q1a.x, q1a.y, q1a.z, q1a.w, q1b.x, q1b.y, q1b.z, q1b.w};
+        float bm0 = p0 + A0.z, bm1 = p1 + A1.z;
+#pragma unroll
+        for (int s = 0; s < 8; ++s) {
+          float z0 = bm0 + c1a[s] * A0.x + c2a[s] * A0.y;
+          float h0 = fmaxf(fmaf(rKa[s], z0, fmaf(-mrKa[s], ws0, A0.w)), 0.f);
+          d8[s] = fmaf(h0, qq0[s], d8[s]);
+          float z1 = bm1 + c1a[s] * A1.x + c2a[s] * A1.y;
+          float h1 = fmaxf(fmaf(rKa[s], z1, fmaf(-mrKa[s], ws1, A1.w)), 0.f);
+          d8[s] = fmaf(h1, qq1[s], d8[s]);
+        }
+      }
+#pragma unroll
+      for (int s = 0; s < 8; ++s) {
+        float v = d8[s];
+        v += __shfl_xor(v, 1, 64);
+        v += __shfl_xor(v, 2, 64);
+        d8[s] = (v + b2qg[b_u * 8 + s]) * 0.125f;
+      }
+      float mx = d8[0];
+#pragma unroll
+      for (int s = 1; s < 8; ++s) mx = fmaxf(mx, d8[s]);
+      float tt = 0.f;
+      float e8[8];
+#pragma unroll
+      for (int s = 0; s < 8; ++s) { e8[s] = expf(d8[s] - mx); tt += e8[s]; }
+      float inv = 1.f / tt;
+#pragma unroll
+      for (int s = 0; s < 8; ++s) e8[s] = e8[s] * inv + 1e-8f;
+      float wa, wb;
+      if (sp == 0) { wa = e8[0]; wb = e8[1]; }
+      else if (sp == 1) { wa = e8[2]; wb = e8[3]; }
+      else if (sp == 2) { wa = e8[4]; wb = e8[5]; }
+      else { wa = e8[6]; wb = e8[7]; }
+      *(float2*)&sm.u.it.attnS[px][sp * 2] = make_float2(wa, wb);
+      if (last) {
+        outAttn[(size_t)(b_u * 8 + sp * 2) * 4096 + jimg] = wa;
+        outAttn[(size_t)(b_u * 8 + sp * 2 + 1) * 4096 + jimg] = wb;
+      }
+      {
+        float mm[10] = {wa, wa * gx, wa * gy, wa * gx * gx, wa * gy * gy,
+                        wb, wb * gx, wb * gy, wb * gx * gx, wb * gy * gy};
+#pragma unroll
+        for (int i = 0; i < 10; ++i) {
+          float v = mm[i];
+          v += __shfl_xor(v, 4, 64); v += __shfl_xor(v, 8, 64);
+          v += __shfl_xor(v, 16, 64); v += __shfl_xor(v, 32, 64);
+          mm[i] = v;
+        }
+        if ((tid & 63) < 4) {
+#pragma unroll
+          for (int i = 0; i < 5; ++i) {
+            atomicAdd(&sm.u.it.momAcc[sp * 2][i], mm[i]);
+            atomicAdd(&sm.u.it.momAcc[sp * 2 + 1][i], mm[5 + i]);
+          }
+        }
+      }
+      __syncthreads();
+
+      if (!last) {
+        const int w = tid >> 6, l = tid & 63;
+        float hacc[8][2];
+#pragma unroll
+        for (int s = 0; s < 8; ++s) { hacc[s][0] = 0.f; hacc[s][1] = 0.f; }
+        const unsigned short* P16 = (const unsigned short*)sm.P0vl[u];
 #pragma unroll 2
-    for (int i = 0; i < 16; ++i) {
-      int j = w * 16 + i;
-      float pv0 = __uint_as_float((unsigned)P16[j * 130 + l] << 16);
-      float pv1 = __uint_as_float((unsigned)P16[j * 130 + 64 + l] << 16);
-      float bm0 = pv0 + ncv0.z, bm1 = pv1 + ncv1.z;
-#pragma unroll
-      for (int s = 0; s < 8; ++s) {
-        float4 sc = scalV[j][s];
-        float aw = attnS[j][s];
-        float z0 = bm0 + sc.x * ncv0.x + sc.y * ncv0.y;
-        float h0 = fmaxf(fmaf(sc.z, z0, fmaf(-sc.w, wsv0, ncv0.w)), 0.f);
-        hacc[s][0] = fmaf(aw, h0, hacc[s][0]);
-        float z1 = bm1 + sc.x * ncv1.x + sc.y * ncv1.y;
-        float h1 = fmaxf(fmaf(sc.z, z1, fmaf(-sc.w, wsv1, ncv1.w)), 0.f);
-        hacc[s][1] = fmaf(aw, h1, hacc[s][1]);
-      }
-    }
-#pragma unroll
-    for (int s = 0; s < 8; ++s) {
-      HsumW[w][s][l] = hacc[s][0];
-      HsumW[w][s][l + 64] = hacc[s][1];
-    }
-    __syncthreads();
-#pragma unroll
-    for (int r = 0; r < 4; ++r) {
-      int i = tid + 256 * r;
-      int s = i >> 7, n = i & 127;
-      float v = HsumW[0][s][n] + HsumW[1][s][n] + HsumW[2][s][n] + HsumW[3][s][n];
-      atomicAdd(&Hsum[(b * 8 + s) * 128 + n], v);
-    }
-  }
-  if (tid < 40)
-    atomicAdd(&moments[(b * 8 + tid / 5) * 5 + tid % 5], momAcc[tid / 5][tid % 5]);
-}
-
-__global__ __launch_bounds__(192) void k_fin(
-    float* __restrict__ moments, float* __restrict__ Hsum,
-    const float* __restrict__ W2, const float* __restrict__ b2,
-    const float* __restrict__ W_ih, const float* __restrict__ b_ih,
-    const float* __restrict__ W_hh, const float* __restrict__ b_hh,
-    const float* __restrict__ g_pre, const float* __restrict__ b_pre,
-    const float* __restrict__ Wf1, const float* __restrict__ bf1,
-    const float* __restrict__ Wf2, const float* __restrict__ bf2,
-    const float* __restrict__ g_slots, const float* __restrict__ b_slots,
-    const float* __restrict__ Wq, const float* __restrict__ bq,
-    float* __restrict__ slotsS, float* __restrict__ sposS, float* __restrict__ sscaleS,
-    float* __restrict__ w2qg, float* __restrict__ b2qg,
-    float* __restrict__ outSlots, float* __restrict__ outSpos,
-    float* __restrict__ outSscale, int last) {
-  const int bs = blockIdx.x;
-  const int t = threadIdx.x;
-  __shared__ float hsum_s[128], upd[64], sprev[64], xg[192], hg[192];
-  __shared__ float snew[64], xpre[64], hf[128], sfin[64], xn[64], qsh[64];
-  const float M0 = moments[bs * 5 + 0];
-  const float M1x = moments[bs * 5 + 1], M1y = moments[bs * 5 + 2];
-  const float M2x = moments[bs * 5 + 3], M2y = moments[bs * 5 + 4];
-  const float invM0 = 1.f / M0;
-  const float spx = M1x * invM0, spy = M1y * invM0;
-  const float M0a = M0 + 4096.f * 1e-8f;
-  const float G2 = 1408.6772487f * 1e-8f;
-  const float vx = (M2x + G2 - 2.f * spx * M1x + spx * spx * M0a) / M0a;
-  const float vy = (M2y + G2 - 2.f * spy * M1y + spy * spy * M0a) / M0a;
-  float ssx = sqrtf(fmaxf(vx, 0.f)), ssy = sqrtf(fmaxf(vy, 0.f));
-  ssx = fminf(fmaxf(ssx, 0.001f), 2.f);
-  ssy = fminf(fmaxf(ssy, 0.001f), 2.f);
-  if (t == 0) {
-    sposS[bs * 2 + 0] = spx; sposS[bs * 2 + 1] = spy;
-    sscaleS[bs * 2 + 0] = ssx; sscaleS[bs * 2 + 1] = ssy;
-    if (last) {
-      outSpos[bs * 2 + 0] = spx; outSpos[bs * 2 + 1] = spy;
-      outSscale[bs * 2 + 0] = ssx; outSscale[bs * 2 + 1] = ssy;
-    }
-  }
-  if (last) {
-    if (t < 64) outSlots[bs * 64 + t] = slotsS[bs * 64 + t];
-    return;
-  }
-  if (t < 128) hsum_s[t] = Hsum[bs * 128 + t];
-  if (t < 64) sprev[t] = slotsS[bs * 64 + t];
-  __syncthreads();
-  if (t < 128) Hsum[bs * 128 + t] = 0.f;
-  if (t < 5) moments[bs * 5 + t] = 0.f;
-  if (t < 64) {
-    float a = 0.f;
-#pragma unroll
-    for (int k = 0; k < 128; ++k) a += hsum_s[k] * W2[k * 64 + t];
-    upd[t] = a * invM0 + b2[t];
-  }
-  __syncthreads();
-  {
-    float a = b_ih[t], h = b_hh[t];
-#pragma unroll
-    for (int d = 0; d < 64; ++d) {
-      a += upd[d] * W_ih[d * 192 + t];
-      h += sprev[d] * W_hh[d * 192 + t];
-    }
-    xg[t] = a; hg[t] = h;
-  }
-  __syncthreads();
-  if (t < 64) {
-    float r = 1.f / (1.f + expf(-(xg[t] + hg[t])));
-    float z = 1.f / (1.f + expf(-(xg[64 + t] + hg[64 + t])));
-    float n = tanhf(xg[128 + t] + r * hg[128 + t]);
-    snew[t] = (1.f - z) * n + z * sprev[t];
-  }
-  __syncthreads();
-  if (t < 64) {
-    float v = snew[t];
-    float m = wave_sum(v) * 0.015625f;
-    float c = v - m;
-    float var = wave_sum(c * c) * 0.015625f;
-    xpre[t] = c * rsqrtf(var + 1e-5f) * g_pre[t] + b_pre[t];
-  }
-  __syncthreads();
-  if (t < 128) {
-    float a = bf1[t];
-#pragma unroll
-    for (int d = 0; d < 64; ++d) a += xpre[d] * Wf1[d * 128 + t];
-    hf[t] = fmaxf(a, 0.f);
-  }
-  __syncthreads();
-  if (t < 64) {
-    float a = bf2[t];
-#pragma unroll
-    for (int k = 0; k < 128; ++k) a += hf[k] * Wf2[k * 64 + t];
-    float nv = snew[t] + a;
-    slotsS[bs * 64 + t] = nv;
-    sfin[t] = nv;
-  }
-  __syncthreads();
-  if (t < 64) {
-    float v = sfin[t];
-    float m = wave_sum(v) * 0.015625f;
-    float c = v - m;
-    float var = wave_sum(c * c) * 0.015625f;
-    xn[t] = c * rsqrtf(var + 1e-5f) * g_slots[t] + b_slots[t];
-  }
-  __syncthreads();
-  if (t < 64) {
-    float a = bq[t];
-#pragma unroll
-    for (int d = 0; d < 64; ++d) a += xn[d] * Wq[d * 64 + t];
-    qsh[t] = a;
-  }
-  __syncthreads();
-  if (t < 128) {
-    float a = 0.f;
-#pragma unroll
-    for (int d = 0; d < 64; ++d) a += W2[t * 64 + d] * qsh[d];
-    w2qg[bs * 128 + t] = a;
-  }
-  if (t < 64) {
-    float p = wave_sum(b2[t] * qsh[t]);
-    if (t == 0) b2qg[bs] = p;
+        for (int i = 0; i < 16; ++i) {
+          int j = w * 16 + i;
+          float pv0 = __uint_as_float((unsigned)P16[j * 130 + l] << 16);
+          float pv1 = __uint_as_float((unsigned)P16[j * 130 + 64 + l] << 16);
+          float bm0 = pv0 + ncv0.z, bm1 = pv1 + ncv1.z;
+#pragma unroll
+          for (int s = 0; s < 8; ++s) {
+            float4 sc = sm.u.it.scalV[j][s];
+            float aw = sm.u.it.attnS[j][s];
+            float z0 = bm0 + sc.x * ncv0.x + sc.y * ncv0.y;
+            float h0 = fmaxf(fmaf(sc.z, z0, fmaf(-sc.w, wsv0, ncv0.w)), 0.f);
+            hacc[s][0] = fmaf(aw, h0, hacc[s][0]);
+            float z1 = bm1 + sc.x * ncv1.x + sc.y * ncv1.y;
+            float h1 = fmaxf(fmaf(sc.z, z1, fmaf(-sc.w, wsv1, ncv1.w)), 0.f);
+            hacc[s][1] = fmaf(aw, h1, hacc[s][1]);
+          }
+        }
+#pragma unroll
+        for (int s = 0; s < 8; ++s) {
+          sm.u.it.HsumW[w][s][l] = hacc[s][0];
+          sm.u.it.HsumW[w][s][l + 64] = hacc[s][1];
+        }
+        __syncthreads();
+#pragma unroll
+        for (int r = 0; r < 4; ++r) {
+          int i = tid + 256 * r;
+          int s = i >> 7, n = i & 127;
+          float v = sm.u.it.HsumW[0][s][n] + sm.u.it.HsumW[1][s][n] +
+                    sm.u.it.HsumW[2][s][n] + sm.u.it.HsumW[3][s][n];
+          atomicAdd(&Hsum[(b_u * 8 + s) * 128 + n], v);
+        }
+      }
+      if (tid < 40)
+        atomicAdd(&moments[(b_u * 8 + tid / 5) * 5 + tid % 5],
+                  sm.u.it.momAcc[tid / 5][tid % 5]);
+      __syncthreads();
+    }
+
+    gbar(&bar[(2 + 2 * itn) * 16]);
+
+    if (bid < 64) {
+      const int bs = bid;
+      const int t = tid;
+      FinS& F = sm.u.it.fin;
+      const float M0 = moments[bs * 5 + 0];
+      const float M1x = moments[bs * 5 + 1], M1y = moments[bs * 5 + 2];
+      const float M2x = moments[bs * 5 + 3], M2y = moments[bs * 5 + 4];
+      const float invM0 = 1.f / M0;
+      const float spx = M1x * invM0, spy = M1y * invM0;
+      const float M0a = M0 + 4096.f * 1e-8f;
+      const float G2 = 1408.6772487f * 1e-8f;
+      const float vx = (M2x + G2 - 2.f * spx * M1x + spx * spx * M0a) / M0a;
+      const float vy = (M2y + G2 - 2.f * spy * M1y + spy * spy * M0a) / M0a;
+      float ssx = sqrtf(fmaxf(vx, 0.f)), ssy = sqrtf(fmaxf(vy, 0.f));
+      ssx = fminf(fmaxf(ssx, 0.001f), 2.f);
+      ssy = fminf(fmaxf(ssy, 0.001f), 2.f);
+      if (t == 0) {
+        sposS[bs * 2 + 0] = spx; sposS[bs * 2 + 1] = spy;
+        sscaleS[bs * 2 + 0] = ssx; sscaleS[bs * 2 + 1] = ssy;
+        if (last) {
+          outSpos[bs * 2 + 0] = spx; outSpos[bs * 2 + 1] = spy;
+          outSscale[bs * 2 + 0] = ssx; outSscale[bs * 2 + 1] = ssy;
+        }
+      }
+      if (last) {
+        if (t < 64) outSlots[bs * 64 + t] = slotsS[bs * 64 + t];
+      } else {
+        if (t < 128) F.hsum_s[t] = Hsum[bs * 128 + t];
+        if (t < 64) F.sprev[t] = slotsS[bs * 64 + t];
+        __syncthreads();
+        if (t < 128) Hsum[bs * 128 + t] = 0.f;
+        if (t < 5) moments[bs * 5 + t] = 0.f;
+        if (t < 64) {
+          float a = 0.f;
+#pragma unroll
+          for (int k = 0; k < 128; ++k) a += F.hsum_s[k] * W2[k * 64 + t];
+          F.upd[t] = a * invM0 + b2[t];
+        }
+        __syncthreads();
+        if (t < 192) {
+          float a = b_ih[t], h = b_hh[t];
+#pragma unroll
+          for (int d = 0; d < 64; ++d) {
+            a += F.upd[d] * W_ih[d * 192 + t];
+            h += F.sprev[d] * W_hh[d * 192 + t];
+          }
+          F.xg[t] = a; F.hg[t] = h;
+        }
+        __syncthreads();
+        if (t < 64) {
+          float r = 1.f / (1.f + expf(-(F.xg[t] + F.hg[t])));
+          float z = 1.f / (1.f + expf(-(F.xg[64 + t] + F.hg[64 + t])));
+          float n = tanhf(F.xg[128 + t] + r * F.hg[128 + t]);
+          F.snew[t] = (1.f - z) * n + z * F.sprev[t];
+        }
+        __syncthreads();
+        if (t < 64) {
+          float v = F.snew[t];
+          float m = wave_sum(v) * 0.015625f;
+          float c = v - m;
+          float var = wave_sum(c * c) * 0.015625f;
+          F.xpre[t] = c * rsqrtf(var + 1e-5f) * g_pre[t] + b_pre[t];
+        }
+        __syncthreads();
+        if (t < 128) {
+          float a = bf1[t];
+#pragma unroll
+          for (int d = 0; d < 64; ++d) a += F.xpre[d] * Wf1[d * 128 + t];
+          F.hf[t] = fmaxf(a, 0.f);
+        }
+        __syncthreads();
+        if (t < 64) {
+          float a = bf2[t];
+#pragma unroll
+          for (int k = 0; k < 128; ++k) a += F.hf[k] * Wf2[k * 64 + t];
+          float nv = F.snew[t] + a;
+          slotsS[bs * 64 + t] = nv;
+          F.sfin[t] = nv;
+        }
+        __syncthreads();
+        if (t < 64) {
+          float v = F.sfin[t];
+          float m = wave_sum(v) * 0.015625f;
+          float c = v - m;
+          float var = wave_sum(c * c) * 0.015625f;
+          F.xn[t] = c * rsqrtf(var + 1e-5f) * g_slots[t] + b_slots[t];
+        }
+        __syncthreads();
+        if (t < 64) {
+          float a = bq[t];
+#pragma unroll
+          for (int d = 0; d < 64; ++d) a += F.xn[d] * Wq[d * 64 + t];
+          F.qsh[t] = a;
+        }
+        __syncthreads();
+        if (t < 128) {
+          float a = 0.f;
+#pragma unroll
+          for (int d = 0; d < 64; ++d) a += W2[t * 64 + d] * F.qsh[d];
+          w2qg[bs * 128 + t] = a;
+        }
+        if (t < 64) {
+          float p = wave_sum(b2[t] * F.qsh[t]);
+          if (t == 0) b2qg[bs] = p;
+        }
+      }
+    }
   }
 }
 
 extern "C" void kernel_launch(void* const* d_in, const int* in_sizes, int n_in,
                               void* d_out, int out_size, void* d_ws, size_t ws_size,
                               hipStream_t stream) {
+  (void)in_sizes; (void)n_in; (void)out_size; (void)ws_size;
   const float* const* in = (const float* const*)d_in;
-  float* ws = (float*)d_ws;
-  bf16_t* P0k   = (bf16_t*)(ws + 0);
-  bf16_t* P0v   = (bf16_t*)(ws + 2097152);
-  float* statsK = ws + 4194304;
-  float* statsV = ws + 4358144;
-  float* w2qg   = ws + 4521984;
-  float* b2qg   = ws + 4530176;
-  float* slotsS = ws + 4530240;
-  float* sposS  = ws + 4534336;
-  float* sscaleS= ws + 4534464;
-  float* moments= ws + 4534592;
-  float* Hsum   = ws + 4534912;
-  bf16_t* W1kT  = (bf16_t*)(ws + 4543104);
-  bf16_t* W1vT  = (bf16_t*)(ws + 4547200);
-  bf16_t* WkT   = (bf16_t*)(ws + 4551296);
-  bf16_t* WvT   = (bf16_t*)(ws + 4553344);
-  float4* nckA  = (float4*)(ws + 4555392);
-  float* nckB   = ws + 4555904;
-  float4* ncvA  = (float4*)(ws + 4556032);
-  float* ncvB   = ws + 4556544;
-  float* possum = ws + 4556672;
-
+  float* wsp = (float*)d_ws;
   float* out = (float*)d_out;
-  float* outSlots  = out;
-  float* outSpos   = out + 4096;
-  float* outSscale = out + 4224;
-  float* outAttn   = out + 4352;
-
-  k_setup<<<1, 256, 0, stream>>>(in[1], in[2], in[3], in[20], in[21],
-                                 in[16], in[17], in[18], in[19], in[4], in[5],
-                                 in[8], in[10], slotsS, sposS, sscaleS, moments,
-                                 W1kT, W1vT, WkT, WvT, nckA, nckB, ncvA, ncvB, possum);
-  k_pre<<<512, 256, 0, stream>>>(in[0], in[12], in[13], in[9], in[11],
-                                 WkT, WvT, W1kT, W1vT, in[4], in[5],
-                                 P0k, P0v, statsK, statsV,
-                                 slotsS, in[14], in[15], in[6], in[7], in[22], in[23],
-                                 w2qg, b2qg);
-  for (int i = 0; i < 4; ++i) {
-    int last = (i == 3) ? 1 : 0;
-    if (!last) {
-      k_iter<0><<<dim3(64, 8), 256, 0, stream>>>(
-          P0k, P0v, statsK, statsV, nckA, nckB, ncvA, ncvB, possum,
-          w2qg, b2qg, sposS, sscaleS, moments, Hsum, outAttn);
-    } else {
-      k_iter<1><<<dim3(64, 8), 256, 0, stream>>>(
-          P0k, P0v, statsK, statsV, nckA, nckB, ncvA, ncvB, possum,
-          w2qg, b2qg, sposS, sscaleS, moments, Hsum, outAttn);
-    }
-    k_fin<<<64, 192, 0, stream>>>(moments, Hsum, in[22], in[23], in[24], in[25],
-                                  in[26], in[27], in[28], in[29], in[30], in[31],
-                                  in[32], in[33], in[14], in[15], in[6], in[7],
-                                  slotsS, sposS, sscaleS, w2qg, b2qg,
-                                  outSlots, outSpos, outSscale, last);
-  }
+  float* oSlots = out;
+  float* oSpos = out + 4096;
+  float* oSscale = out + 4224;
+  float* oAttn = out + 4352;
+
+  hipMemsetAsync((char*)d_ws + 139264, 0, 576, stream);
+
+  k_fused<<<NBLK, 256, 0, stream>>>(
+      in[0], in[1], in[2], in[3], in[4], in[5], in[6], in[7], in[8], in[9],
+      in[10], in[11], in[12], in[13], in[14], in[15], in[16], in[17], in[18],
+      in[19], in[20], in[21], in[22], in[23], in[24], in[25], in[26], in[27],
+      in[28], in[29], in[30], in[31], in[32], in[33],
+      wsp, oSlots, oSpos, oSscale, oAttn);
 }
```

New measurement: 880.9 us. 2.93x slower.
